# Kernel optimization log

Measured on AMD Instinct MI355X. Metric: run time of the kernel, lower is better.

The kernel has to match this reference:

```python
import jax, jax.numpy as jnp
import numpy as np

D = 192
HEADS = 4
HD = D // HEADS
R = 3  # correlation radius actually used in forward_level
NDISP = (2 * R + 1) ** 2  # 49
T = 3  # frames -> 2 consecutive pairs
ITERS = 4


def layer_norm(x, w, b, eps=1e-5):
    m = jnp.mean(x, axis=-1, keepdims=True)
    v = jnp.var(x, axis=-1, keepdims=True)
    return (x - m) / jnp.sqrt(v + eps) * w + b


def mha(x, in_w, in_b, out_w, out_b):
    # torch nn.MultiheadAttention, batch_first, self-attention
    B, N, _ = x.shape
    qkv = x @ in_w.T + in_b
    q, k, v = jnp.split(qkv, 3, axis=-1)
    q = q.reshape(B, N, HEADS, HD).transpose(0, 2, 1, 3) * (1.0 / float(np.sqrt(HD)))
    k = k.reshape(B, N, HEADS, HD).transpose(0, 2, 1, 3)
    v = v.reshape(B, N, HEADS, HD).transpose(0, 2, 1, 3)
    att = jax.nn.softmax(jnp.einsum('bhqd,bhkd->bhqk', q, k), axis=-1)
    y = jnp.einsum('bhqk,bhkd->bhqd', att, v).transpose(0, 2, 1, 3).reshape(B, N, D)
    return y @ out_w.T + out_b


def tblock(x, p):
    ln1w, ln1b, inw, inb, ow, ob, ln2w, ln2b, w1, b1, w2, b2 = p
    x = x + mha(layer_norm(x, ln1w, ln1b), inw, inb, ow, ob)
    h = layer_norm(x, ln2w, ln2b)
    h = jax.nn.gelu(h @ w1.T + b1, approximate=False) @ w2.T + b2
    return x + h


def local_corr(f1, f2):
    C = f1.shape[1]
    scale = 1.0 / float(np.sqrt(C))
    outs = []
    for dy in range(-R, R + 1):
        for dx in range(-R, R + 1):
            f2s = jnp.roll(f2, (dy, dx), axis=(2, 3))
            outs.append(jnp.sum(f1 * f2s, axis=1) * scale)
    return jnp.stack(outs, axis=1)


def grid_sample_bilinear_border(img, grid):
    # img: B,C,H,W; grid: B,Ho,Wo,2 with (x,y) in [-1,1]; align_corners=True, border padding
    B, C, H, W = img.shape
    x = jnp.clip((grid[..., 0] + 1.0) * 0.5 * (W - 1), 0.0, W - 1)
    y = jnp.clip((grid[..., 1] + 1.0) * 0.5 * (H - 1), 0.0, H - 1)
    x0 = jnp.floor(x); y0 = jnp.floor(y)
    x1 = jnp.minimum(x0 + 1, W - 1); y1 = jnp.minimum(y0 + 1, H - 1)
    wx = (x - x0)[:, None]; wy = (y - y0)[:, None]
    imgf = img.reshape(B, C, H * W)
    Ho, Wo = x.shape[1], x.shape[2]
    def gather(yy, xx):
        idx = (yy * W + xx).astype(jnp.int32).reshape(B, 1, Ho * Wo)
        return jnp.take_along_axis(imgf, idx, axis=2).reshape(B, C, Ho, Wo)
    v00 = gather(y0, x0); v01 = gather(y0, x1)
    v10 = gather(y1, x0); v11 = gather(y1, x1)
    return v00 * (1 - wx) * (1 - wy) + v01 * wx * (1 - wy) + v10 * (1 - wx) * wy + v11 * wx * wy


def warp(img, flow):
    # flow in pixels, Bx2xHxW
    B, C, H, W = img.shape
    xs = jnp.linspace(-1.0, 1.0, W); ys = jnp.linspace(-1.0, 1.0, H)
    gx, gy = jnp.meshgrid(xs, ys)  # each (H, W), 'xy' indexing
    base = jnp.stack([gx, gy], axis=-1)[None]
    off = jnp.stack([flow[:, 0] * (2.0 / max(W - 1, 1)),
                     flow[:, 1] * (2.0 / max(H - 1, 1))], axis=-1)
    return grid_sample_bilinear_border(img, base + off)


def upsample2x_align(img):
    # F.interpolate(scale_factor=2, mode='bilinear', align_corners=True)
    B, C, H, W = img.shape
    Ho, Wo = 2 * H, 2 * W
    xs = jnp.linspace(-1.0, 1.0, Wo); ys = jnp.linspace(-1.0, 1.0, Ho)
    gx, gy = jnp.meshgrid(xs, ys)
    grid = jnp.broadcast_to(jnp.stack([gx, gy], axis=-1)[None], (B, Ho, Wo, 2))
    return grid_sample_bilinear_border(img, grid)


def conv2d(x, w, b):
    y = jax.lax.conv_general_dilated(x, w, (1, 1), ((1, 1), (1, 1)),
                                     dimension_numbers=('NCHW', 'OIHW', 'NCHW'))
    return y + b[None, :, None, None]


def _forward(feats_l1, feats_l2, feats_l3, tok_w, tok_b,
             lcm_ln1_w, lcm_ln1_b, lcm_in_w, lcm_in_b, lcm_out_w, lcm_out_b,
             lcm_ln2_w, lcm_ln2_b, lcm_mlp_w1, lcm_mlp_b1, lcm_mlp_w2, lcm_mlp_b2,
             gtr_ln1_w, gtr_ln1_b, gtr_in_w, gtr_in_b, gtr_out_w, gtr_out_b,
             gtr_ln2_w, gtr_ln2_b, gtr_mlp_w1, gtr_mlp_b1, gtr_mlp_w2, gtr_mlp_b2,
             head_w1, head_b1, head_w2, head_b2,
             ref1_w1, ref1_b1, ref1_w2, ref1_b2,
             ref0_w1, ref0_b1, ref0_w2, ref0_b2):
    feats = [[feats_l1[t] for t in range(T)],
             [feats_l2[t] for t in range(T)],
             [feats_l3[t] for t in range(T)]]
    # ---- CostTokenizer ----
    tokens = []
    for lvl in range(3):
        toks = []
        for k in range(T - 1):
            corr = local_corr(feats[lvl][k], feats[lvl][k + 1])
            toks.append(jnp.einsum('bchw,dc->bdhw', corr, tok_w[lvl]) + tok_b[lvl][None, :, None, None])
        tokens.append(toks)
    lcm_p = [(lcm_ln1_w[i], lcm_ln1_b[i], lcm_in_w[i], lcm_in_b[i], lcm_out_w[i], lcm_out_b[i],
              lcm_ln2_w[i], lcm_ln2_b[i], lcm_mlp_w1[i], lcm_mlp_b1[i], lcm_mlp_w2[i], lcm_mlp_b2[i])
             for i in range(lcm_ln1_w.shape[0])]
    gtr_p = [(gtr_ln1_w[i], gtr_ln1_b[i], gtr_in_w[i], gtr_in_b[i], gtr_out_w[i], gtr_out_b[i],
              gtr_ln2_w[i], gtr_ln2_b[i], gtr_mlp_w1[i], gtr_mlp_b1[i], gtr_mlp_w2[i], gtr_mlp_b2[i])
             for i in range(gtr_ln1_w.shape[0])]
    # ---- LatentCostMemory (EMA state; .detach() -> stop_gradient; state resets when N changes) ----
    state = None
    latent = []
    for toks in tokens:
        lvl_lat = []
        for tok in toks:
            B_, Dd, H, W = tok.shape
            x = tok.reshape(B_, Dd, H * W).transpose(0, 2, 1)  # b (h w) d
            for p in lcm_p:
                x = tblock(x, p)
            if state is None or state.shape[1] != x.shape[1]:
                state = jax.lax.stop_gradient(x)
            x = 0.8 * x + 0.2 * state
            state = jax.lax.stop_gradient(x)
            lvl_lat.append(x.transpose(0, 2, 1))  # b d n
        latent.append(lvl_lat)
    H8, W8 = feats[1][0].shape[-2:]
    coarse = []
    for lat in latent[1]:
        x = lat.transpose(0, 2, 1)
        for p in gtr_p:
            x = tblock(x, p)
        fv = jax.nn.gelu(x @ head_w1.T + head_b1, approximate=False) @ head_w2.T + head_b2
        coarse.append(fv.transpose(0, 2, 1).reshape(-1, 2, H8, W8))
    # ---- MSRecurrentDecoder ----
    outs = []
    for k, f8 in enumerate(coarse):
        cur = f8
        for _ in range(ITERS):
            w10 = warp(feats[1][k + 1], cur)
            x = jnp.concatenate([feats[1][k], cur, w10], axis=1)
            cur = cur + conv2d(jax.nn.gelu(conv2d(x, ref1_w1, ref1_b1), approximate=False), ref1_w2, ref1_b2)
        cur2 = upsample2x_align(cur)
        for _ in range(ITERS):
            w10 = warp(feats[0][k + 1], cur2)
            x = jnp.concatenate([feats[0][k], cur2, w10], axis=1)
            cur2 = cur2 + conv2d(jax.nn.gelu(conv2d(x, ref0_w1, ref0_b1), approximate=False), ref0_w2, ref0_b2)
        outs.append(cur2)
    return jnp.stack(outs)  # [pairs, B, 2, H/4, W/4]


def setup_inputs():
    key = jax.random.key(0)
    ks = iter(jax.random.split(key, 64))
    def rn(shape, s=1.0):
        return jax.random.normal(next(ks), shape, dtype=jnp.float32) * s
    B = 1
    inp = {}
    inp['feats_l1'] = rn((T, B, 64, 64, 64))
    inp['feats_l2'] = rn((T, B, 128, 32, 32))
    inp['feats_l3'] = rn((T, B, 192, 16, 16))
    inp['tok_w'] = rn((3, D, NDISP), 0.02)
    inp['tok_b'] = rn((3, D), 0.02)
    for pre, n in (('lcm', 6), ('gtr', 2)):
        inp[pre + '_ln1_w'] = jnp.ones((n, D), jnp.float32)
        inp[pre + '_ln1_b'] = jnp.zeros((n, D), jnp.float32)
        inp[pre + '_in_w'] = rn((n, 3 * D, D), 0.02)
        inp[pre + '_in_b'] = rn((n, 3 * D), 0.02)
        inp[pre + '_out_w'] = rn((n, D, D), 0.02)
        inp[pre + '_out_b'] = rn((n, D), 0.02)
        inp[pre + '_ln2_w'] = jnp.ones((n, D), jnp.float32)
        inp[pre + '_ln2_b'] = jnp.zeros((n, D), jnp.float32)
        inp[pre + '_mlp_w1'] = rn((n, 4 * D, D), 0.02)
        inp[pre + '_mlp_b1'] = rn((n, 4 * D), 0.02)
        inp[pre + '_mlp_w2'] = rn((n, D, 4 * D), 0.02)
        inp[pre + '_mlp_b2'] = rn((n, D), 0.02)
    inp['head_w1'] = rn((D, D), 0.02); inp['head_b1'] = rn((D,), 0.02)
    inp['head_w2'] = rn((2, D), 0.02); inp['head_b2'] = rn((2,), 0.02)
    inp['ref1_w1'] = rn((128, 258, 3, 3), 0.02); inp['ref1_b1'] = rn((128,), 0.02)
    inp['ref1_w2'] = rn((2, 128, 3, 3), 0.02); inp['ref1_b2'] = rn((2,), 0.02)
    inp['ref0_w1'] = rn((64, 130, 3, 3), 0.02); inp['ref0_b1'] = rn((64,), 0.02)
    inp['ref0_w2'] = rn((2, 64, 3, 3), 0.02); inp['ref0_b2'] = rn((2,), 0.02)
    return inp


def reference(feats_l1, feats_l2, feats_l3, tok_w, tok_b,
              lcm_ln1_w, lcm_ln1_b, lcm_in_w, lcm_in_b, lcm_out_w, lcm_out_b,
              lcm_ln2_w, lcm_ln2_b, lcm_mlp_w1, lcm_mlp_b1, lcm_mlp_w2, lcm_mlp_b2,
              gtr_ln1_w, gtr_ln1_b, gtr_in_w, gtr_in_b, gtr_out_w, gtr_out_b,
              gtr_ln2_w, gtr_ln2_b, gtr_mlp_w1, gtr_mlp_b1, gtr_mlp_w2, gtr_mlp_b2,
              head_w1, head_b1, head_w2, head_b2,
              ref1_w1, ref1_b1, ref1_w2, ref1_b2,
              ref0_w1, ref0_b1, ref0_w2, ref0_b2):
    return _forward(feats_l1, feats_l2, feats_l3, tok_w, tok_b,
                    lcm_ln1_w, lcm_ln1_b, lcm_in_w, lcm_in_b, lcm_out_w, lcm_out_b,
                    lcm_ln2_w, lcm_ln2_b, lcm_mlp_w1, lcm_mlp_b1, lcm_mlp_w2, lcm_mlp_b2,
                    gtr_ln1_w, gtr_ln1_b, gtr_in_w, gtr_in_b, gtr_out_w, gtr_out_b,
                    gtr_ln2_w, gtr_ln2_b, gtr_mlp_w1, gtr_mlp_b1, gtr_mlp_w2, gtr_mlp_b2,
                    head_w1, head_b1, head_w2, head_b2,
                    ref1_w1, ref1_b1, ref1_w2, ref1_b2,
                    ref0_w1, ref0_b1, ref0_w2, ref0_b2)
```

## Files before the change

### kernel.cpp

```cpp
#include <hip/hip_runtime.h>
#include <hip/hip_bf16.h>

typedef __hip_bfloat16 bf16;
typedef short bf16x8 __attribute__((ext_vector_type(8)));
typedef float f32x4 __attribute__((ext_vector_type(4)));

#define DEV __device__ __forceinline__

DEV float bf2f(bf16 v) { return __bfloat162float(v); }
DEV bf16 f2bf(float v) { return __float2bfloat16(v); }
DEV unsigned short bfr(float f) {
  bf16 h = __float2bfloat16(f);
  return *reinterpret_cast<unsigned short*>(&h);
}
DEV float shf(unsigned short u) {
  unsigned int x = ((unsigned int)u) << 16;
  return *reinterpret_cast<float*>(&x);
}
DEV float gelu_exact(float x) { return 0.5f * x * (1.0f + erff(x * 0.70710678118654752f)); }

DEV float ldw(const void* p, long i, int isb) {
  return isb ? __bfloat162float(((const bf16*)p)[i]) : ((const float*)p)[i];
}

__global__ void k_detect(const unsigned short* __restrict__ u, int* __restrict__ flag) {
  __shared__ int bad;
  if (threadIdx.x == 0) bad = 0;
  __syncthreads();
  for (int i = threadIdx.x; i < 8192; i += 256) {
    int expo = (u[i] >> 7) & 0xFF;
    if (expo >= 138) atomicOr(&bad, 1);
  }
  __syncthreads();
  if (threadIdx.x == 0) *flag = bad ? 0 : 1;
}
__global__ void k_setone(int* p) { *p = 1; }

__global__ void k_cvt(const void* __restrict__ s, float* __restrict__ d, int n,
                      const int* __restrict__ fl) {
  int isb = *fl;
  int i = blockIdx.x * blockDim.x + threadIdx.x;
  if (i < n) d[i] = ldw(s, i, isb);
}

__global__ void k_zerosh(unsigned short* __restrict__ p, int n8) {
  int i = blockIdx.x * blockDim.x + threadIdx.x;
  if (i < n8) { uint4 z = {0, 0, 0, 0}; *(uint4*)(p + (long)i * 8) = z; }
}

__global__ void k_padtokw(const void* __restrict__ tw, bf16* __restrict__ dst,
                          const int* __restrict__ fl) {
  int isb = *fl;
  int i = blockIdx.x * blockDim.x + threadIdx.x;
  if (i >= 12288) return;
  int n = i >> 6, k = i & 63;
  float v = (k < 49) ? ldw(tw, 9408 + (long)n * 49 + k, isb) : 0.0f;
  dst[i] = f2bf(v);
}

__global__ void k_packw(const void* __restrict__ src, bf16* __restrict__ dst,
                        int OC, int C, int ICT, int NP, int ICP, int n,
                        const int* __restrict__ fl) {
  int isb = *fl;
  int i = blockIdx.x * blockDim.x + threadIdx.x;
  if (i >= n) return;
  int s = i / (NP * ICP);
  int r = i - s * NP * ICP;
  int oc = r / ICP, icp = r - oc * ICP;
  float v = 0.0f;
  if (oc < OC) {
    int ic = -1;
    if (icp < C) ic = icp;
    else if (icp < 2 * C) ic = icp - C + C + 2;
    else if (icp < 2 * C + 2) ic = icp - 2 * C + C;
    if (ic >= 0 && ic < ICT) v = ldw(src, ((long)oc * ICT + ic) * 9 + s, isb);
  }
  dst[i] = f2bf(v);
}

__global__ void k_trans_feats(const void* __restrict__ in, bf16* __restrict__ Fp,
                              int F, int C, int HW, const int* __restrict__ fl) {
  int isb = *fl;
  int cpg = C >> 3;
  int n = F * HW * cpg;
  int i = blockIdx.x * blockDim.x + threadIdx.x;
  if (i >= n) return;
  int p = i % HW;
  int rem = i / HW;
  int c8 = rem % cpg;
  int f = rem / cpg;
  long base = (long)f * C * HW + (long)(c8 * 8) * HW + p;
  union { unsigned short u[8]; uint4 v; } pk;
#pragma unroll
  for (int j = 0; j < 8; ++j) pk.u[j] = bfr(ldw(in, base + (long)j * HW, isb));
  *(uint4*)((unsigned short*)Fp + ((long)f * HW + p) * C + c8 * 8) = pk.v;
}

template <int C, int ICP, int NOUT, int WW, int LGW>
__global__ __launch_bounds__(256) void k_conv_warp2(
    const bf16* __restrict__ Fp, const float* __restrict__ flow,
    const bf16* __restrict__ Wp, const float* __restrict__ bias,
    bf16* __restrict__ out) {
  constexpr int HH = WW;
  constexpr int HW = HH * WW;
  constexpr int ACW = 34;
  constexpr int AR = 3 * ACW;
  constexpr int NK = ICP / 32;
  constexpr int NWI = 5;
  __shared__ unsigned short Asm[AR][40];
  __shared__ unsigned short Wsm[9 * 32][40];
  int tid = threadIdx.x;
  int wv = tid >> 6, ln = tid & 63, quad = ln >> 4, l16 = ln & 15;
  int wm = wv & 1, wn = wv >> 1;
  int n0 = blockIdx.x * 32, m0 = blockIdx.y * 32, b = blockIdx.z;
  int py0 = m0 >> LGW, px0 = m0 & (WW - 1);
  const unsigned short* fcur = (const unsigned short*)Fp + (long)b * HW * C;
  const unsigned short* fnxt = (const unsigned short*)Fp + (long)(b + 1) * HW * C;
  const float* fl = flow + (long)b * 2 * HW;
  int c4 = tid & 3;
  const uint4 Z4 = {0, 0, 0, 0};
  int rr_[2], ipp[2];
  bool ivalid[2], iin[2];
  float w00[2], w01[2], w10[2], w11[2], ifx[2], ify[2];
  const unsigned short *g00[2], *g01[2], *g10[2], *g11[2];
#pragma unroll
  for (int j = 0; j < 2; ++j) {
    int idx = tid + j * 256;
    ivalid[j] = idx < AR * 4;
    int r = idx >> 2;
    rr_[j] = r;
    int sr = r / ACW, sc = r - sr * ACW;
    int py = py0 + sr - 1, px = px0 + sc - 1;
    bool in = ivalid[j] && py >= 0 && py < HH && px >= 0 && px < WW;
    iin[j] = in;
    int p = in ? (py * WW + px) : 0;
    ipp[j] = p;
    float fx = 0.0f, fy = 0.0f;
    if (in) { fx = fl[p]; fy = fl[HW + p]; }
    ifx[j] = fx; ify[j] = fy;
    float x = fminf(fmaxf((float)px + fx, 0.0f), (float)(WW - 1));
    float y = fminf(fmaxf((float)py + fy, 0.0f), (float)(HH - 1));
    int x0 = (int)floorf(x), y0 = (int)floorf(y);
    int x1 = min(x0 + 1, WW - 1), y1 = min(y0 + 1, HH - 1);
    float wx = x - (float)x0, wy = y - (float)y0;
    w00[j] = (1 - wx) * (1 - wy); w01[j] = wx * (1 - wy);
    w10[j] = (1 - wx) * wy;       w11[j] = wx * wy;
    g00[j] = fnxt + (long)(y0 * WW + x0) * C;
    g01[j] = fnxt + (long)(y0 * WW + x1) * C;
    g10[j] = fnxt + (long)(y1 * WW + x0) * C;
    g11[j] = fnxt + (long)(y1 * WW + x1) * C;
  }
  uint4 fa[2] = {};
  uint4 qa[2], qb[2], qc[2], qd[2];
  uint4 wreg[NWI];
  auto ldW = [&](int kc) {
#pragma unroll
    for (int j = 0; j < NWI; ++j) {
      int idx = tid + j * 256;
      if (idx < 9 * 32 * 4) {
        int r = idx >> 2, cw = idx & 3;
        int s = r >> 5, nl = r & 31;
        wreg[j] = *(const uint4*)((const unsigned short*)Wp +
                                  ((long)s * NOUT + n0 + nl) * ICP + kc * 32 + cw * 8);
      }
    }
  };
  auto stW = [&]() {
#pragma unroll
    for (int j = 0; j < NWI; ++j) {
      int idx = tid + j * 256;
      if (idx < 9 * 32 * 4) {
        int r = idx >> 2, cw = idx & 3;
        *(uint4*)&Wsm[r][cw * 8] = wreg[j];
      }
    }
  };
  auto ldA = [&](int kc) {
    int chb = kc * 32;
    if (chb < C) {
#pragma unroll
      for (int j = 0; j < 2; ++j) {
        if (iin[j]) fa[j] = *(const uint4*)(fcur + (long)ipp[j] * C + chb + c4 * 8);
        else fa[j] = Z4;
      }
    } else if (chb < 2 * C) {
      int c = chb - C + c4 * 8;
#pragma unroll
      for (int j = 0; j < 2; ++j) {
        if (iin[j]) {
          qa[j] = *(const uint4*)(g00[j] + c);
          qb[j] = *(const uint4*)(g01[j] + c);
          qc[j] = *(const uint4*)(g10[j] + c);
          qd[j] = *(const uint4*)(g11[j] + c);
        }
      }
    }
  };
  auto stA = [&](int kc) {
    int chb = kc * 32;
    if (chb < C) {
#pragma unroll
      for (int j = 0; j < 2; ++j)
        if (ivalid[j]) *(uint4*)&Asm[rr_[j]][c4 * 8] = fa[j];
    } else if (chb < 2 * C) {
#pragma unroll
      for (int j = 0; j < 2; ++j) {
        if (!ivalid[j]) continue;
        uint4 val = Z4;
        if (iin[j]) {
          union { unsigned short u[8]; uint4 v; } A_ = { .v = qa[j] };
          union { unsigned short u[8]; uint4 v; } B_ = { .v = qb[j] };
          union { unsigned short u[8]; uint4 v; } C_ = { .v = qc[j] };
          union { unsigned short u[8]; uint4 v; } D_ = { .v = qd[j] };
          union { unsigned short u[8]; uint4 v; } O_;
#pragma unroll
          for (int e = 0; e < 8; ++e)
            O_.u[e] = bfr(shf(A_.u[e]) * w00[j] + shf(B_.u[e]) * w01[j] +
                          shf(C_.u[e]) * w10[j] + shf(D_.u[e]) * w11[j]);
          val = O_.v;
        }
        *(uint4*)&Asm[rr_[j]][c4 * 8] = val;
      }
    } else {
#pragma unroll
      for (int j = 0; j < 2; ++j) {
        if (!ivalid[j]) continue;
        union { unsigned short u[8]; uint4 v; } O_ = { .v = {0, 0, 0, 0} };
        if (iin[j] && c4 == 0) { O_.u[0] = bfr(ifx[j]); O_.u[1] = bfr(ify[j]); }
        *(uint4*)&Asm[rr_[j]][c4 * 8] = O_.v;
      }
    }
  };
  f32x4 acc = {};
  int mml = wm * 16 + l16;
  ldW(0);
  ldA(0);
#pragma unroll
  for (int kc = 0; kc < NK; ++kc) {
    stW();
    stA(kc);
    __syncthreads();
    if (kc + 1 < NK) { ldW(kc + 1); ldA(kc + 1); }
#pragma unroll
    for (int s = 0; s < 9; ++s) {
      int ky = s / 3, kx = s - ky * 3;
      bf16x8 af = *(const bf16x8*)&Asm[ky * ACW + mml + kx][quad * 8];
      bf16x8 wf = *(const bf16x8*)&Wsm[s * 32 + wn * 16 + l16][quad * 8];
      acc = __builtin_amdgcn_mfma_f32_16x16x32_bf16(af, wf, acc, 0, 0, 0);
    }
    __syncthreads();
  }
  int n = n0 + wn * 16 + l16;
  float bv = bias[n];
  constexpr int Wp2 = WW + 2;
#pragma unroll
  for (int r = 0; r < 4; ++r) {
    int mmo = m0 + wm * 16 + quad * 4 + r;
    int py = mmo >> LGW, px = mmo & (WW - 1);
    float v = gelu_exact(acc[r] + bv);
    ((unsigned short*)out)[((long)b * (HH + 2) * Wp2 + (long)(py + 1) * Wp2 + px + 1) * NOUT + n]
        = bfr(v);
  }
}

template <int C, int WW, int LGW>
__global__ __launch_bounds__(256) void k_conv2_dot(
    const bf16* __restrict__ mid, const bf16* __restrict__ Wq,
    const float* __restrict__ bias, float* __restrict__ cur) {
  constexpr int HH = WW;
  constexpr int HW = HH * WW;
  constexpr int Wp2 = WW + 2;
  constexpr int CPL = C / 64;
  int tid = threadIdx.x, wv = tid >> 6, ln = tid & 63;
  int gw = blockIdx.x * 4 + wv;
  int b = gw >> (2 * LGW);
  int p = gw & (HW - 1);
  int py = p >> LGW, px = p & (WW - 1);
  float r0 = cur[((long)b * 2 + 0) * HW + p];
  float r1 = cur[((long)b * 2 + 1) * HW + p];
  float b0 = bias[0], b1 = bias[1];
  const unsigned short* base = (const unsigned short*)mid +
      ((long)b * (HH + 2) * Wp2 + (long)py * Wp2 + px) * C + ln * CPL;
  const unsigned short* wb = (const unsigned short*)Wq + ln * CPL;
  float s0 = 0.0f, s1 = 0.0f;
#pragma unroll
  for (int t = 0; t < 9; ++t) {
    int dy = t / 3, dx = t - dy * 3;
    const unsigned short* ar = base + ((long)dy * Wp2 + dx) * C;
    const unsigned short* w0r = wb + (long)(t * 16 + 0) * C;
    const unsigned short* w1r = wb + (long)(t * 16 + 1) * C;
    if (CPL == 2) {
      unsigned int a = *(const unsigned int*)ar;
      unsigned int q0 = *(const unsigned int*)w0r;
      unsigned int q1 = *(const unsigned int*)w1r;
      float a0 = shf((unsigned short)a), a1 = shf((unsigned short)(a >> 16));
      s0 += a0 * shf((unsigned short)q0) + a1 * shf((unsigned short)(q0 >> 16));
      s1 += a0 * shf((unsigned short)q1) + a1 * shf((unsigned short)(q1 >> 16));
    } else {
      float a0 = shf(ar[0]);
      s0 += a0 * shf(w0r[0]);
      s1 += a0 * shf(w1r[0]);
    }
  }
#pragma unroll
  for (int o = 32; o; o >>= 1) { s0 += __shfl_xor(s0, o); s1 += __shfl_xor(s1, o); }
  if (ln == 0) {
    cur[((long)b * 2 + 0) * HW + p] = s0 + b0 + r0;
    cur[((long)b * 2 + 1) * HW + p] = s1 + b1 + r1;
  }
}

__global__ void k_corr(const bf16* __restrict__ Fp2, bf16* __restrict__ corrT) {
  __shared__ unsigned short f1r[128];
  int p = blockIdx.x;
  int b = blockIdx.y;
  int t = threadIdx.x;
  const unsigned short* f1 = (const unsigned short*)Fp2 + ((long)b * 1024 + p) * 128;
  if (t < 16) *(uint4*)&f1r[t * 8] = *(const uint4*)(f1 + t * 8);
  __syncthreads();
  long rowo = ((long)b * 1024 + p) * 64;
  if (t < 49) {
    int dy = t / 7 - 3, dx = t % 7 - 3;
    int h = p >> 5, w = p & 31;
    int p2 = (((h - dy) & 31) << 5) | ((w - dx) & 31);
    const unsigned short* f2 = (const unsigned short*)Fp2 + ((long)(b + 1) * 1024 + p2) * 128;
    float s = 0.0f;
    for (int c = 0; c < 128; c += 8) {
      union { unsigned short u[8]; uint4 v; } av = { .v = *(const uint4*)&f1r[c] };
      union { unsigned short u[8]; uint4 v; } bv = { .v = *(const uint4*)(f2 + c) };
#pragma unroll
      for (int j = 0; j < 8; ++j) s += shf(av.u[j]) * shf(bv.u[j]);
    }
    corrT[rowo + t] = f2bf(s * 0.08838834764831845f);
  } else {
    corrT[rowo + t] = f2bf(0.0f);
  }
}

template <int KT, int BM, int ACT, bool HASRES, int AMODE, int OUTBF, int VT>
__global__ __launch_bounds__(256) void k_gemm_mfma2(
    const void* __restrict__ A, const void* __restrict__ W, long woff,
    const void* __restrict__ bias, long boff, const int* __restrict__ flb,
    const float* __restrict__ res, void* __restrict__ C,
    int M, int N, const int* __restrict__ fl,
// ... 375 lines not shown
  bf16* w0p1 = (bf16*)(wpk + 175104);
  bf16* w0p2 = (bf16*)(wpk + 221184);

  float* x = rX;
  bf16* corrTb = (bf16*)big;
  bf16* qkvbb  = (bf16*)big;
  bf16* vtb    = (bf16*)(big + 655360);
  bf16* hidb   = (bf16*)big;
  unsigned short* opart = (unsigned short*)rA;
  float* mlbuf = rY;
  float* headh = rT;
  bf16* mid0p = (bf16*)rT;
  bf16* mid1p = (bf16*)rY;
  bf16* Fp2   = (bf16*)(big + 851968);
  bf16* Fp1   = (bf16*)(big + 1048576);

  k_detect<<<1, 256, 0, stream>>>((const unsigned short*)feats_l1, flag);
  k_setone<<<1, 1, 0, stream>>>(oneflag);
  k_cvt<<<1, 256, 0, stream>>>(ref1_b1, cb1a, 128, flag);
  k_cvt<<<1, 256, 0, stream>>>(ref1_b2, cb1b, 2, flag);
  k_cvt<<<1, 256, 0, stream>>>(ref0_b1, cb0a, 64, flag);
  k_cvt<<<1, 256, 0, stream>>>(ref0_b2, cb0b, 2, flag);
  k_padtokw<<<48, 256, 0, stream>>>(tok_w, wtok, flag);
  k_packw<<<1296, 256, 0, stream>>>(ref1_w1, w1p1, 128, 128, 258, 128, 288, 331776, flag);
  k_packw<<<72, 256, 0, stream>>>(ref1_w2, w1p2, 2, 128, 128, 16, 128, 18432, flag);
  k_packw<<<360, 256, 0, stream>>>(ref0_w1, w0p1, 64, 64, 130, 64, 160, 92160, flag);
  k_packw<<<36, 256, 0, stream>>>(ref0_w2, w0p2, 2, 64, 64, 16, 64, 9216, flag);
  k_trans_feats<<<192, 256, 0, stream>>>(feats_l2, Fp2, 3, 128, 1024, flag);
  k_trans_feats<<<384, 256, 0, stream>>>(feats_l1, Fp1, 3, 64, 4096, flag);

  k_corr<<<dim3(1024, 2), 64, 0, stream>>>(Fp2, corrTb);
  k_gemm_mfma2<64, 32, 0, false, 1, 0, 0><<<dim3(3, 64), 256, 0, stream>>>(
      corrTb, wtok, 0, tok_b, 192, flag, nullptr, x, 2048, 192, oneflag,
      nullptr, nullptr, nullptr, nullptr, 0, nullptr, 0);

  auto run_block = [&](const void* ln1w, long o1, const void* ln1b, long o2,
                       const void* inw, long o3, const void* inb, long o4,
                       const void* ow, long o5, const void* ob, long o6,
                       const void* ln2w, long o7, const void* ln2b, long o8,
                       const void* w1, long o9, const void* b1, long o10,
                       const void* w2, long o11, const void* b2, long o12) {
    k_gemm_mfma2<192, 64, 0, false, 3, 1, 1><<<dim3(9, 32), 256, 0, stream>>>(
        x, inw, o3, inb, o4, flag, nullptr, qkvbb, 2048, 576, flag,
        nullptr, nullptr, vtb, ln1w, o1, ln1b, o2);
    k_attn_mfma<<<dim3(64, 4, 2), 256, 0, stream>>>(qkvbb, vtb, opart, mlbuf);
    k_gemm_mfma2<192, 32, 0, true, 2, 0, 0><<<dim3(3, 64), 256, 0, stream>>>(
        nullptr, ow, o5, ob, o6, flag, x, x, 2048, 192, flag,
        opart, mlbuf, nullptr, nullptr, 0, nullptr, 0);
    k_gemm_mfma2<192, 64, 1, false, 3, 1, 0><<<dim3(12, 32), 256, 0, stream>>>(
        x, w1, o9, b1, o10, flag, nullptr, hidb, 2048, 768, flag,
        nullptr, nullptr, nullptr, ln2w, o7, ln2b, o8);
    k_gemm_mfma2<768, 32, 0, true, 1, 0, 0><<<dim3(3, 64), 256, 0, stream>>>(
        hidb, w2, o11, b2, o12, flag, x, x, 2048, 192, flag,
        nullptr, nullptr, nullptr, nullptr, 0, nullptr, 0);
  };

  for (int i = 0; i < 6; ++i) {
    run_block(lcm_ln1_w, (long)i * 192, lcm_ln1_b, (long)i * 192,
              lcm_in_w, (long)i * 110592, lcm_in_b, (long)i * 576,
              lcm_out_w, (long)i * 36864, lcm_out_b, (long)i * 192,
              lcm_ln2_w, (long)i * 192, lcm_ln2_b, (long)i * 192,
              lcm_mlp_w1, (long)i * 147456, lcm_mlp_b1, (long)i * 768,
              lcm_mlp_w2, (long)i * 147456, lcm_mlp_b2, (long)i * 192);
  }
  k_ema<<<768, 256, 0, stream>>>(x);

  for (int i = 0; i < 2; ++i) {
    run_block(gtr_ln1_w, (long)i * 192, gtr_ln1_b, (long)i * 192,
              gtr_in_w, (long)i * 110592, gtr_in_b, (long)i * 576,
              gtr_out_w, (long)i * 36864, gtr_out_b, (long)i * 192,
              gtr_ln2_w, (long)i * 192, gtr_ln2_b, (long)i * 192,
              gtr_mlp_w1, (long)i * 147456, gtr_mlp_b1, (long)i * 768,
              gtr_mlp_w2, (long)i * 147456, gtr_mlp_b2, (long)i * 192);
  }

  k_gemm_mfma2<192, 32, 1, false, 0, 0, 0><<<dim3(3, 64), 256, 0, stream>>>(
      x, head_w1, 0, head_b1, 0, flag, nullptr, headh, 2048, 192, flag,
      nullptr, nullptr, nullptr, nullptr, 0, nullptr, 0);
  k_head2<<<1024, 256, 0, stream>>>(headh, head_w2, head_b2, cur, flag);

  k_zerosh<<<768, 256, 0, stream>>>((unsigned short*)rT, 196608);

  for (int it = 0; it < 4; ++it) {
    k_conv_warp2<128, 288, 128, 32, 5><<<dim3(4, 32, 2), 256, 0, stream>>>(
        Fp2, cur, w1p1, cb1a, mid1p);
    k_conv2_dot<128, 32, 5><<<512, 256, 0, stream>>>(mid1p, w1p2, cb1b, cur);
  }
  k_upsample<<<64, 256, 0, stream>>>(cur, cur2);

  for (int it = 0; it < 4; ++it) {
    k_conv_warp2<64, 160, 64, 64, 6><<<dim3(2, 128, 2), 256, 0, stream>>>(
        Fp1, cur2, w0p1, cb0a, mid0p);
    k_conv2_dot<64, 64, 6><<<2048, 256, 0, stream>>>(mid0p, w0p2, cb0b, cur2);
  }

  k_out<<<64, 256, 0, stream>>>(cur2, d_out, flag);
}
```

Before: 1.008 ms.

## Stage full input channel patch once in LDS for warped 3x3 conv

```diff
diff --git a/kernel.cpp b/kernel.cpp
--- a/kernel.cpp
+++ b/kernel.cpp
@@ -96,168 +96,162 @@
   *(uint4*)((unsigned short*)Fp + ((long)f * HW + p) * C + c8 * 8) = pk.v;
 }
 
-template <int C, int ICP, int NOUT, int WW, int LGW>
-__global__ __launch_bounds__(256) void k_conv_warp2(
+template <int C, int ICP, int ICPP, int NOUT, int WW, int LGW>
+__global__ __launch_bounds__(256) void k_conv_osa(
     const bf16* __restrict__ Fp, const float* __restrict__ flow,
     const bf16* __restrict__ Wp, const float* __restrict__ bias,
     bf16* __restrict__ out) {
-  constexpr int HH = WW;
-  constexpr int HW = HH * WW;
-  constexpr int ACW = 34;
-  constexpr int AR = 3 * ACW;
+  constexpr int HH = WW, HW = WW * WW;
+  constexpr int CW = (WW < 64) ? WW : 64;
+  constexpr int LGCW = (CW == 64) ? 6 : 5;
+  constexpr int RO = 64 / CW;
+  constexpr int ACW = CW + 2;
+  constexpr int APX = (RO + 2) * ACW;
   constexpr int NK = ICP / 32;
-  constexpr int NWI = 5;
-  __shared__ unsigned short Asm[AR][40];
-  __shared__ unsigned short Wsm[9 * 32][40];
+  constexpr int CG = C / 8;
+  constexpr int NFEAT = APX * CG;
+  constexpr int NFI = (NFEAT + 255) / 256;
+  constexpr int TG = (ICP - 2 * C) / 8;
+  __shared__ unsigned short As[APX][ICPP];
+  __shared__ unsigned short Ws[2][144][40];
+  __shared__ int doff[APX][4];
+  __shared__ float dwt[APX][4];
   int tid = threadIdx.x;
   int wv = tid >> 6, ln = tid & 63, quad = ln >> 4, l16 = ln & 15;
-  int wm = wv & 1, wn = wv >> 1;
-  int n0 = blockIdx.x * 32, m0 = blockIdx.y * 32, b = blockIdx.z;
-  int py0 = m0 >> LGW, px0 = m0 & (WW - 1);
+  int n0 = blockIdx.x * 16, m0 = blockIdx.y * 64, b = blockIdx.z;
+  int py0 = m0 >> LGW;
   const unsigned short* fcur = (const unsigned short*)Fp + (long)b * HW * C;
   const unsigned short* fnxt = (const unsigned short*)Fp + (long)(b + 1) * HW * C;
   const float* fl = flow + (long)b * 2 * HW;
-  int c4 = tid & 3;
-  const uint4 Z4 = {0, 0, 0, 0};
-  int rr_[2], ipp[2];
-  bool ivalid[2], iin[2];
-  float w00[2], w01[2], w10[2], w11[2], ifx[2], ify[2];
-  const unsigned short *g00[2], *g01[2], *g10[2], *g11[2];
-#pragma unroll
-  for (int j = 0; j < 2; ++j) {
-    int idx = tid + j * 256;
-    ivalid[j] = idx < AR * 4;
-    int r = idx >> 2;
-    rr_[j] = r;
-    int sr = r / ACW, sc = r - sr * ACW;
-    int py = py0 + sr - 1, px = px0 + sc - 1;
-    bool in = ivalid[j] && py >= 0 && py < HH && px >= 0 && px < WW;
-    iin[j] = in;
+  uint4 wrg[3];
+  auto ldWs = [&](int kc) {
+#pragma unroll
+    for (int j = 0; j < 3; ++j) {
+      int i = tid + j * 256;
+      if (i < 576) {
+        int r = i >> 2, c4 = i & 3;
+        int s = r >> 4, nl = r & 15;
+        wrg[j] = *(const uint4*)((const unsigned short*)Wp +
+                 ((long)s * NOUT + n0 + nl) * ICP + kc * 32 + c4 * 8);
+      }
+    }
+  };
+  auto stWs = [&](int bsel) {
+#pragma unroll
+    for (int j = 0; j < 3; ++j) {
+      int i = tid + j * 256;
+      if (i < 576) {
+        int r = i >> 2, c4 = i & 3;
+        *(uint4*)&Ws[bsel][r][c4 * 8] = wrg[j];
+      }
+    }
+  };
+  uint4 fva[NFI];
+  int fap[NFI], fcg[NFI];
+  bool fok[NFI];
+#pragma unroll
+  for (int j = 0; j < NFI; ++j) {
+    int i = tid + j * 256;
+    bool v = i < NFEAT;
+    int ap = v ? (i / CG) : 0;
+    int cg = i & (CG - 1);
+    fap[j] = ap; fcg[j] = cg; fok[j] = v;
+    int sr = ap / ACW, sc = ap - sr * ACW;
+    int py = py0 + sr - 1, px = sc - 1;
+    bool in = v && py >= 0 && py < HH && px >= 0 && px < WW;
+    uint4 z = {0, 0, 0, 0};
+    fva[j] = in ? *(const uint4*)(fcur + (long)(py * WW + px) * C + cg * 8) : z;
+  }
+  ldWs(0);
+  if (tid < APX) {
+    int ap = tid;
+    int sr = ap / ACW, sc = ap - sr * ACW;
+    int py = py0 + sr - 1, px = sc - 1;
+    bool in = py >= 0 && py < HH && px >= 0 && px < WW;
     int p = in ? (py * WW + px) : 0;
-    ipp[j] = p;
-    float fx = 0.0f, fy = 0.0f;
-    if (in) { fx = fl[p]; fy = fl[HW + p]; }
-    ifx[j] = fx; ify[j] = fy;
+    float fx = in ? fl[p] : 0.0f, fy = in ? fl[HW + p] : 0.0f;
     float x = fminf(fmaxf((float)px + fx, 0.0f), (float)(WW - 1));
     float y = fminf(fmaxf((float)py + fy, 0.0f), (float)(HH - 1));
     int x0 = (int)floorf(x), y0 = (int)floorf(y);
     int x1 = min(x0 + 1, WW - 1), y1 = min(y0 + 1, HH - 1);
     float wx = x - (float)x0, wy = y - (float)y0;
-    w00[j] = (1 - wx) * (1 - wy); w01[j] = wx * (1 - wy);
-    w10[j] = (1 - wx) * wy;       w11[j] = wx * wy;
-    g00[j] = fnxt + (long)(y0 * WW + x0) * C;
-    g01[j] = fnxt + (long)(y0 * WW + x1) * C;
-    g10[j] = fnxt + (long)(y1 * WW + x0) * C;
-    g11[j] = fnxt + (long)(y1 * WW + x1) * C;
-  }
-  uint4 fa[2] = {};
-  uint4 qa[2], qb[2], qc[2], qd[2];
-  uint4 wreg[NWI];
-  auto ldW = [&](int kc) {
-#pragma unroll
-    for (int j = 0; j < NWI; ++j) {
-      int idx = tid + j * 256;
-      if (idx < 9 * 32 * 4) {
-        int r = idx >> 2, cw = idx & 3;
-        int s = r >> 5, nl = r & 31;
-        wreg[j] = *(const uint4*)((const unsigned short*)Wp +
-                                  ((long)s * NOUT + n0 + nl) * ICP + kc * 32 + cw * 8);
-      }
-    }
-  };
-  auto stW = [&]() {
-#pragma unroll
-    for (int j = 0; j < NWI; ++j) {
-      int idx = tid + j * 256;
-      if (idx < 9 * 32 * 4) {
-        int r = idx >> 2, cw = idx & 3;
-        *(uint4*)&Wsm[r][cw * 8] = wreg[j];
-      }
-    }
-  };
-  auto ldA = [&](int kc) {
-    int chb = kc * 32;
-    if (chb < C) {
-#pragma unroll
-      for (int j = 0; j < 2; ++j) {
-        if (iin[j]) fa[j] = *(const uint4*)(fcur + (long)ipp[j] * C + chb + c4 * 8);
-        else fa[j] = Z4;
-      }
-    } else if (chb < 2 * C) {
-      int c = chb - C + c4 * 8;
-#pragma unroll
-      for (int j = 0; j < 2; ++j) {
-        if (iin[j]) {
-          qa[j] = *(const uint4*)(g00[j] + c);
-          qb[j] = *(const uint4*)(g01[j] + c);
-          qc[j] = *(const uint4*)(g10[j] + c);
-          qd[j] = *(const uint4*)(g11[j] + c);
-        }
-      }
-    }
-  };
-  auto stA = [&](int kc) {
-    int chb = kc * 32;
-    if (chb < C) {
-#pragma unroll
-      for (int j = 0; j < 2; ++j)
-        if (ivalid[j]) *(uint4*)&Asm[rr_[j]][c4 * 8] = fa[j];
-    } else if (chb < 2 * C) {
-#pragma unroll
-      for (int j = 0; j < 2; ++j) {
-        if (!ivalid[j]) continue;
-        uint4 val = Z4;
-        if (iin[j]) {
-          union { unsigned short u[8]; uint4 v; } A_ = { .v = qa[j] };
-          union { unsigned short u[8]; uint4 v; } B_ = { .v = qb[j] };
-          union { unsigned short u[8]; uint4 v; } C_ = { .v = qc[j] };
-          union { unsigned short u[8]; uint4 v; } D_ = { .v = qd[j] };
-          union { unsigned short u[8]; uint4 v; } O_;
-#pragma unroll
-          for (int e = 0; e < 8; ++e)
-            O_.u[e] = bfr(shf(A_.u[e]) * w00[j] + shf(B_.u[e]) * w01[j] +
-                          shf(C_.u[e]) * w10[j] + shf(D_.u[e]) * w11[j]);
-          val = O_.v;
-        }
-        *(uint4*)&Asm[rr_[j]][c4 * 8] = val;
-      }
-    } else {
-#pragma unroll
-      for (int j = 0; j < 2; ++j) {
-        if (!ivalid[j]) continue;
-        union { unsigned short u[8]; uint4 v; } O_ = { .v = {0, 0, 0, 0} };
-        if (iin[j] && c4 == 0) { O_.u[0] = bfr(ifx[j]); O_.u[1] = bfr(ify[j]); }
-        *(uint4*)&Asm[rr_[j]][c4 * 8] = O_.v;
-      }
-    }
-  };
-  f32x4 acc = {};
-  int mml = wm * 16 + l16;
-  ldW(0);
-  ldA(0);
-#pragma unroll
+    float q00 = in ? (1 - wx) * (1 - wy) : 0.0f, q01 = in ? wx * (1 - wy) : 0.0f;
+    float q10 = in ? (1 - wx) * wy : 0.0f,       q11 = in ? wx * wy : 0.0f;
+    doff[ap][0] = (y0 * WW + x0) * C; doff[ap][1] = (y0 * WW + x1) * C;
+    doff[ap][2] = (y1 * WW + x0) * C; doff[ap][3] = (y1 * WW + x1) * C;
+    dwt[ap][0] = q00; dwt[ap][1] = q01; dwt[ap][2] = q10; dwt[ap][3] = q11;
+#pragma unroll
+    for (int t = 0; t < TG; ++t) {
+      union { unsigned short u[8]; uint4 v; } o = { .v = {0, 0, 0, 0} };
+      if (t == 0 && in) { o.u[0] = bfr(fx); o.u[1] = bfr(fy); }
+      *(uint4*)&As[ap][2 * C + t * 8] = o.v;
+    }
+  }
+#pragma unroll
+  for (int j = 0; j < NFI; ++j)
+    if (fok[j]) *(uint4*)&As[fap[j]][fcg[j] * 8] = fva[j];
+  stWs(0);
+  __syncthreads();
+#pragma unroll
+  for (int jc = 0; jc < (NFI + 2) / 3; ++jc) {
+    uint4 q[3][4];
+    float w4[3][4];
+    int ga[3], gc[3];
+    bool gv[3];
+#pragma unroll
+    for (int u = 0; u < 3; ++u) {
+      int j = jc * 3 + u;
+      int i = tid + j * 256;
+      bool v = (j < NFI) && (i < NFEAT);
+      gv[u] = v;
+      int ap = v ? (i / CG) : 0;
+      int cg = i & (CG - 1);
+      ga[u] = ap; gc[u] = cg;
+#pragma unroll
+      for (int e = 0; e < 4; ++e) {
+        w4[u][e] = dwt[ap][e];
+        q[u][e] = *(const uint4*)(fnxt + doff[ap][e] + cg * 8);
+      }
+    }
+#pragma unroll
+    for (int u = 0; u < 3; ++u) {
+      if (!gv[u]) continue;
+      union { unsigned short s[8]; uint4 v; } a0 = {.v = q[u][0]}, a1 = {.v = q[u][1]},
+                                              a2 = {.v = q[u][2]}, a3 = {.v = q[u][3]}, o;
+#pragma unroll
+      for (int e = 0; e < 8; ++e)
+        o.s[e] = bfr(shf(a0.s[e]) * w4[u][0] + shf(a1.s[e]) * w4[u][1] +
+                     shf(a2.s[e]) * w4[u][2] + shf(a3.s[e]) * w4[u][3]);
+      *(uint4*)&As[ga[u]][C + gc[u] * 8] = o.v;
+    }
+  }
+  __syncthreads();
+  int pl = wv * 16 + l16;
+  int prow = pl >> LGCW, pcol = pl & (CW - 1);
+  f32x4 ac0 = {}, ac1 = {}, ac2 = {};
   for (int kc = 0; kc < NK; ++kc) {
-    stW();
-    stA(kc);
-    __syncthreads();
-    if (kc + 1 < NK) { ldW(kc + 1); ldA(kc + 1); }
+    if (kc + 1 < NK) ldWs(kc + 1);
+    int cb = kc & 1;
 #pragma unroll
     for (int s = 0; s < 9; ++s) {
       int ky = s / 3, kx = s - ky * 3;
-      bf16x8 af = *(const bf16x8*)&Asm[ky * ACW + mml + kx][quad * 8];
-      bf16x8 wf = *(const bf16x8*)&Wsm[s * 32 + wn * 16 + l16][quad * 8];
-      acc = __builtin_amdgcn_mfma_f32_16x16x32_bf16(af, wf, acc, 0, 0, 0);
-    }
+      bf16x8 af = *(const bf16x8*)&As[(prow + ky) * ACW + pcol + kx][kc * 32 + quad * 8];
+      bf16x8 wf = *(const bf16x8*)&Ws[cb][s * 16 + l16][quad * 8];
+      if (s % 3 == 0)      ac0 = __builtin_amdgcn_mfma_f32_16x16x32_bf16(af, wf, ac0, 0, 0, 0);
+      else if (s % 3 == 1) ac1 = __builtin_amdgcn_mfma_f32_16x16x32_bf16(af, wf, ac1, 0, 0, 0);
+      else                 ac2 = __builtin_amdgcn_mfma_f32_16x16x32_bf16(af, wf, ac2, 0, 0, 0);
+    }
+    if (kc + 1 < NK) stWs((kc + 1) & 1);
     __syncthreads();
   }
-  int n = n0 + wn * 16 + l16;
+  int n = n0 + l16;
   float bv = bias[n];
   constexpr int Wp2 = WW + 2;
 #pragma unroll
   for (int r = 0; r < 4; ++r) {
-    int mmo = m0 + wm * 16 + quad * 4 + r;
-    int py = mmo >> LGW, px = mmo & (WW - 1);
-    float v = gelu_exact(acc[r] + bv);
+    int pix = m0 + wv * 16 + quad * 4 + r;
+    int py = pix >> LGW, px = pix & (WW - 1);
+    float v = gelu_exact(ac0[r] + ac1[r] + ac2[r] + bv);
     ((unsigned short*)out)[((long)b * (HH + 2) * Wp2 + (long)(py + 1) * Wp2 + px + 1) * NOUT + n]
         = bfr(v);
   }
@@ -801,14 +795,14 @@
   k_zerosh<<<768, 256, 0, stream>>>((unsigned short*)rT, 196608);
 
   for (int it = 0; it < 4; ++it) {
-    k_conv_warp2<128, 288, 128, 32, 5><<<dim3(4, 32, 2), 256, 0, stream>>>(
+    k_conv_osa<128, 288, 296, 128, 32, 5><<<dim3(8, 16, 2), 256, 0, stream>>>(
         Fp2, cur, w1p1, cb1a, mid1p);
     k_conv2_dot<128, 32, 5><<<512, 256, 0, stream>>>(mid1p, w1p2, cb1b, cur);
   }
   k_upsample<<<64, 256, 0, stream>>>(cur, cur2);
 
   for (int it = 0; it < 4; ++it) {
-    k_conv_warp2<64, 160, 64, 64, 6><<<dim3(2, 128, 2), 256, 0, stream>>>(
+    k_conv_osa<64, 160, 168, 64, 64, 6><<<dim3(4, 64, 2), 256, 0, stream>>>(
         Fp1, cur2, w0p1, cb0a, mid0p);
     k_conv2_dot<64, 64, 6><<<2048, 256, 0, stream>>>(mid0p, w0p2, cb0b, cur2);
   }
```

Measured after the change: 1.160 ms. 1.15x slower.

## Shrink warp-conv kernel to single-wave 16x16 tiles with shared warp metadata

Applied to the files above, without the earlier changes.

```diff
diff --git a/kernel.cpp b/kernel.cpp
--- a/kernel.cpp
+++ b/kernel.cpp
@@ -96,102 +96,91 @@
   *(uint4*)((unsigned short*)Fp + ((long)f * HW + p) * C + c8 * 8) = pk.v;
 }
 
-template <int C, int ICP, int NOUT, int WW, int LGW>
-__global__ __launch_bounds__(256) void k_conv_warp2(
+template <int C, int ICP, int NP, int WW, int LGW>
+__global__ __launch_bounds__(64) void k_conv1w(
     const bf16* __restrict__ Fp, const float* __restrict__ flow,
     const bf16* __restrict__ Wp, const float* __restrict__ bias,
     bf16* __restrict__ out) {
-  constexpr int HH = WW;
-  constexpr int HW = HH * WW;
-  constexpr int ACW = 34;
-  constexpr int AR = 3 * ACW;
+  constexpr int HH = WW, HW = WW * WW;
+  constexpr int ACW = 18, APX = 54;
   constexpr int NK = ICP / 32;
-  constexpr int NWI = 5;
-  __shared__ unsigned short Asm[AR][40];
-  __shared__ unsigned short Wsm[9 * 32][40];
-  int tid = threadIdx.x;
-  int wv = tid >> 6, ln = tid & 63, quad = ln >> 4, l16 = ln & 15;
-  int wm = wv & 1, wn = wv >> 1;
-  int n0 = blockIdx.x * 32, m0 = blockIdx.y * 32, b = blockIdx.z;
+  __shared__ unsigned short As[APX][40];
+  __shared__ unsigned short Ws[144][40];
+  __shared__ int pofs[APX];
+  __shared__ int doff[APX][4];
+  __shared__ float dwt[APX][4];
+  __shared__ float ffl[APX][2];
+  int ln = threadIdx.x;
+  int quad = ln >> 4, l16 = ln & 15;
+  int n0 = blockIdx.x * 16, m0 = blockIdx.y * 16, b = blockIdx.z;
   int py0 = m0 >> LGW, px0 = m0 & (WW - 1);
   const unsigned short* fcur = (const unsigned short*)Fp + (long)b * HW * C;
   const unsigned short* fnxt = (const unsigned short*)Fp + (long)(b + 1) * HW * C;
   const float* fl = flow + (long)b * 2 * HW;
-  int c4 = tid & 3;
-  const uint4 Z4 = {0, 0, 0, 0};
-  int rr_[2], ipp[2];
-  bool ivalid[2], iin[2];
-  float w00[2], w01[2], w10[2], w11[2], ifx[2], ify[2];
-  const unsigned short *g00[2], *g01[2], *g10[2], *g11[2];
-#pragma unroll
-  for (int j = 0; j < 2; ++j) {
-    int idx = tid + j * 256;
-    ivalid[j] = idx < AR * 4;
-    int r = idx >> 2;
-    rr_[j] = r;
-    int sr = r / ACW, sc = r - sr * ACW;
+  if (ln < APX) {
+    int sr = ln / ACW, sc = ln - sr * ACW;
     int py = py0 + sr - 1, px = px0 + sc - 1;
-    bool in = ivalid[j] && py >= 0 && py < HH && px >= 0 && px < WW;
-    iin[j] = in;
+    bool in = py >= 0 && py < HH && px >= 0 && px < WW;
     int p = in ? (py * WW + px) : 0;
-    ipp[j] = p;
-    float fx = 0.0f, fy = 0.0f;
-    if (in) { fx = fl[p]; fy = fl[HW + p]; }
-    ifx[j] = fx; ify[j] = fy;
+    pofs[ln] = in ? p * C : -1;
+    float fx = in ? fl[p] : 0.0f, fy = in ? fl[HW + p] : 0.0f;
     float x = fminf(fmaxf((float)px + fx, 0.0f), (float)(WW - 1));
     float y = fminf(fmaxf((float)py + fy, 0.0f), (float)(HH - 1));
     int x0 = (int)floorf(x), y0 = (int)floorf(y);
     int x1 = min(x0 + 1, WW - 1), y1 = min(y0 + 1, HH - 1);
     float wx = x - (float)x0, wy = y - (float)y0;
-    w00[j] = (1 - wx) * (1 - wy); w01[j] = wx * (1 - wy);
-    w10[j] = (1 - wx) * wy;       w11[j] = wx * wy;
-    g00[j] = fnxt + (long)(y0 * WW + x0) * C;
-    g01[j] = fnxt + (long)(y0 * WW + x1) * C;
-    g10[j] = fnxt + (long)(y1 * WW + x0) * C;
-    g11[j] = fnxt + (long)(y1 * WW + x1) * C;
-  }
-  uint4 fa[2] = {};
-  uint4 qa[2], qb[2], qc[2], qd[2];
-  uint4 wreg[NWI];
+    dwt[ln][0] = in ? (1 - wx) * (1 - wy) : 0.0f;
+    dwt[ln][1] = in ? wx * (1 - wy) : 0.0f;
+    dwt[ln][2] = in ? (1 - wx) * wy : 0.0f;
+    dwt[ln][3] = in ? wx * wy : 0.0f;
+    doff[ln][0] = (y0 * WW + x0) * C; doff[ln][1] = (y0 * WW + x1) * C;
+    doff[ln][2] = (y1 * WW + x0) * C; doff[ln][3] = (y1 * WW + x1) * C;
+    ffl[ln][0] = in ? fx : 0.0f; ffl[ln][1] = in ? fy : 0.0f;
+  }
+  uint4 wrg[9];
+  uint4 arg[4];
+  uint4 qrg[4][4];
   auto ldW = [&](int kc) {
 #pragma unroll
-    for (int j = 0; j < NWI; ++j) {
-      int idx = tid + j * 256;
-      if (idx < 9 * 32 * 4) {
-        int r = idx >> 2, cw = idx & 3;
-        int s = r >> 5, nl = r & 31;
-        wreg[j] = *(const uint4*)((const unsigned short*)Wp +
-                                  ((long)s * NOUT + n0 + nl) * ICP + kc * 32 + cw * 8);
-      }
+    for (int j = 0; j < 9; ++j) {
+      int idx = ln + j * 64;
+      int r = idx >> 2, c4 = idx & 3;
+      int s = r >> 4, nl = r & 15;
+      wrg[j] = *(const uint4*)((const unsigned short*)Wp +
+               ((long)s * NP + n0 + nl) * ICP + kc * 32 + c4 * 8);
     }
   };
   auto stW = [&]() {
 #pragma unroll
-    for (int j = 0; j < NWI; ++j) {
-      int idx = tid + j * 256;
-      if (idx < 9 * 32 * 4) {
-        int r = idx >> 2, cw = idx & 3;
-        *(uint4*)&Wsm[r][cw * 8] = wreg[j];
-      }
+    for (int j = 0; j < 9; ++j) {
+      int idx = ln + j * 64;
+      int r = idx >> 2, c4 = idx & 3;
+      *(uint4*)&Ws[r][c4 * 8] = wrg[j];
     }
   };
   auto ldA = [&](int kc) {
     int chb = kc * 32;
     if (chb < C) {
 #pragma unroll
-      for (int j = 0; j < 2; ++j) {
-        if (iin[j]) fa[j] = *(const uint4*)(fcur + (long)ipp[j] * C + chb + c4 * 8);
-        else fa[j] = Z4;
+      for (int j = 0; j < 4; ++j) {
+        int idx = ln + j * 64;
+        if (idx < APX * 4) {
+          int ap = idx >> 2, c4 = idx & 3;
+          int po = pofs[ap];
+          uint4 z = {0, 0, 0, 0};
+          arg[j] = (po >= 0) ? *(const uint4*)(fcur + po + chb + c4 * 8) : z;
+        }
       }
     } else if (chb < 2 * C) {
-      int c = chb - C + c4 * 8;
-#pragma unroll
-      for (int j = 0; j < 2; ++j) {
-        if (iin[j]) {
-          qa[j] = *(const uint4*)(g00[j] + c);
-          qb[j] = *(const uint4*)(g01[j] + c);
-          qc[j] = *(const uint4*)(g10[j] + c);
-          qd[j] = *(const uint4*)(g11[j] + c);
+#pragma unroll
+      for (int j = 0; j < 4; ++j) {
+        int idx = ln + j * 64;
+        if (idx < APX * 4) {
+          int ap = idx >> 2, c4 = idx & 3;
+          int c = chb - C + c4 * 8;
+#pragma unroll
+          for (int e = 0; e < 4; ++e)
+            qrg[j][e] = *(const uint4*)(fnxt + doff[ap][e] + c);
         }
       }
     }
@@ -200,66 +189,70 @@
     int chb = kc * 32;
     if (chb < C) {
 #pragma unroll
-      for (int j = 0; j < 2; ++j)
-        if (ivalid[j]) *(uint4*)&Asm[rr_[j]][c4 * 8] = fa[j];
+      for (int j = 0; j < 4; ++j) {
+        int idx = ln + j * 64;
+        if (idx < APX * 4) {
+          int ap = idx >> 2, c4 = idx & 3;
+          *(uint4*)&As[ap][c4 * 8] = arg[j];
+        }
+      }
     } else if (chb < 2 * C) {
 #pragma unroll
-      for (int j = 0; j < 2; ++j) {
-        if (!ivalid[j]) continue;
-        uint4 val = Z4;
-        if (iin[j]) {
-          union { unsigned short u[8]; uint4 v; } A_ = { .v = qa[j] };
-          union { unsigned short u[8]; uint4 v; } B_ = { .v = qb[j] };
-          union { unsigned short u[8]; uint4 v; } C_ = { .v = qc[j] };
-          union { unsigned short u[8]; uint4 v; } D_ = { .v = qd[j] };
-          union { unsigned short u[8]; uint4 v; } O_;
+      for (int j = 0; j < 4; ++j) {
+        int idx = ln + j * 64;
+        if (idx < APX * 4) {
+          int ap = idx >> 2, c4 = idx & 3;
+          union { unsigned short u[8]; uint4 v; } a0 = {.v = qrg[j][0]}, a1 = {.v = qrg[j][1]},
+                                                  a2 = {.v = qrg[j][2]}, a3 = {.v = qrg[j][3]}, o;
+          float q0 = dwt[ap][0], q1 = dwt[ap][1], q2 = dwt[ap][2], q3 = dwt[ap][3];
 #pragma unroll
           for (int e = 0; e < 8; ++e)
-            O_.u[e] = bfr(shf(A_.u[e]) * w00[j] + shf(B_.u[e]) * w01[j] +
-                          shf(C_.u[e]) * w10[j] + shf(D_.u[e]) * w11[j]);
-          val = O_.v;
+            o.u[e] = bfr(shf(a0.u[e]) * q0 + shf(a1.u[e]) * q1 +
+                         shf(a2.u[e]) * q2 + shf(a3.u[e]) * q3);
+          *(uint4*)&As[ap][c4 * 8] = o.v;
         }
-        *(uint4*)&Asm[rr_[j]][c4 * 8] = val;
       }
     } else {
 #pragma unroll
-      for (int j = 0; j < 2; ++j) {
-        if (!ivalid[j]) continue;
-        union { unsigned short u[8]; uint4 v; } O_ = { .v = {0, 0, 0, 0} };
-        if (iin[j] && c4 == 0) { O_.u[0] = bfr(ifx[j]); O_.u[1] = bfr(ify[j]); }
-        *(uint4*)&Asm[rr_[j]][c4 * 8] = O_.v;
+      for (int j = 0; j < 4; ++j) {
+        int idx = ln + j * 64;
+        if (idx < APX * 4) {
+          int ap = idx >> 2, c4 = idx & 3;
+          union { unsigned short u[8]; uint4 v; } o = { .v = {0, 0, 0, 0} };
+          if (c4 == 0) { o.u[0] = bfr(ffl[ap][0]); o.u[1] = bfr(ffl[ap][1]); }
+          *(uint4*)&As[ap][c4 * 8] = o.v;
+        }
       }
     }
   };
-  f32x4 acc = {};
-  int mml = wm * 16 + l16;
-  ldW(0);
-  ldA(0);
-#pragma unroll
-  for (int kc = 0; kc < NK; ++kc) {
-    stW();
-    stA(kc);
-    __syncthreads();
-    if (kc + 1 < NK) { ldW(kc + 1); ldA(kc + 1); }
+  f32x4 ac0 = {}, ac1 = {}, ac2 = {};
+  auto mm = [&]() {
 #pragma unroll
     for (int s = 0; s < 9; ++s) {
       int ky = s / 3, kx = s - ky * 3;
-      bf16x8 af = *(const bf16x8*)&Asm[ky * ACW + mml + kx][quad * 8];
-      bf16x8 wf = *(const bf16x8*)&Wsm[s * 32 + wn * 16 + l16][quad * 8];
-      acc = __builtin_amdgcn_mfma_f32_16x16x32_bf16(af, wf, acc, 0, 0, 0);
-    }
-    __syncthreads();
-  }
-  int n = n0 + wn * 16 + l16;
+      bf16x8 af = *(const bf16x8*)&As[ky * ACW + l16 + kx][quad * 8];
+      bf16x8 wf = *(const bf16x8*)&Ws[s * 16 + l16][quad * 8];
+      if (s % 3 == 0)      ac0 = __builtin_amdgcn_mfma_f32_16x16x32_bf16(af, wf, ac0, 0, 0, 0);
+      else if (s % 3 == 1) ac1 = __builtin_amdgcn_mfma_f32_16x16x32_bf16(af, wf, ac1, 0, 0, 0);
+      else                 ac2 = __builtin_amdgcn_mfma_f32_16x16x32_bf16(af, wf, ac2, 0, 0, 0);
+    }
+  };
+  ldW(0); ldA(0);
+  stW(); stA(0);
+#pragma unroll
+  for (int kc = 0; kc < NK; ++kc) {
+    if (kc + 1 < NK) { ldW(kc + 1); ldA(kc + 1); }
+    mm();
+    if (kc + 1 < NK) { stW(); stA(kc + 1); }
+  }
+  int n = n0 + l16;
   float bv = bias[n];
-  constexpr int Wp2 = WW + 2;
+  long rowbase = (long)b * (HH + 2) * (WW + 2) + (long)(py0 + 1) * (WW + 2);
 #pragma unroll
   for (int r = 0; r < 4; ++r) {
-    int mmo = m0 + wm * 16 + quad * 4 + r;
-    int py = mmo >> LGW, px = mmo & (WW - 1);
-    float v = gelu_exact(acc[r] + bv);
-    ((unsigned short*)out)[((long)b * (HH + 2) * Wp2 + (long)(py + 1) * Wp2 + px + 1) * NOUT + n]
-        = bfr(v);
+    int px = px0 + quad * 4 + r;
+    float v = gelu_exact(ac0[r] + ac1[r] + ac2[r] + bv);
+    ((unsigned short*)out)[(rowbase + px + 1) * NP + n] = bfr(v);
   }
 }
 
@@ -801,14 +794,14 @@
   k_zerosh<<<768, 256, 0, stream>>>((unsigned short*)rT, 196608);
 
   for (int it = 0; it < 4; ++it) {
-    k_conv_warp2<128, 288, 128, 32, 5><<<dim3(4, 32, 2), 256, 0, stream>>>(
+    k_conv1w<128, 288, 128, 32, 5><<<dim3(8, 64, 2), 64, 0, stream>>>(
         Fp2, cur, w1p1, cb1a, mid1p);
     k_conv2_dot<128, 32, 5><<<512, 256, 0, stream>>>(mid1p, w1p2, cb1b, cur);
   }
   k_upsample<<<64, 256, 0, stream>>>(cur, cur2);
 
   for (int it = 0; it < 4; ++it) {
-    k_conv_warp2<64, 160, 64, 64, 6><<<dim3(2, 128, 2), 256, 0, stream>>>(
+    k_conv1w<64, 160, 64, 64, 6><<<dim3(4, 256, 2), 64, 0, stream>>>(
         Fp1, cur2, w0p1, cb0a, mid0p);
     k_conv2_dot<64, 64, 6><<<2048, 256, 0, stream>>>(mid0p, w0p2, cb0b, cur2);
   }
```

Result: slower. 1.106 ms (+9.8%).
